# Optimization experiments

Hardware: AMD Instinct MI355X
Metric: run time of the kernel (lower is better)

The kernel has to match this reference:

```python
import jax, jax.numpy as jnp
import numpy as np

N_NODES = 100000
N_EDGES = 1600000
IN_F = 64
H1_F = 64
N_CLS = 16
NEG_SLOPE = 0.01  # F.leaky_relu default


def _sage_pool(x, src, dst, n_nodes, W_pool, b_pool, W_self, W_neigh, bias):
    """DGL SAGEConv with aggregator_type='pool'.
    msg = relu(x[src] @ W_pool + b_pool); pooled = max over in-edges per dst
    out = x @ W_self + pooled @ W_neigh + bias (empty segments pooled to 0)."""
    m = jax.nn.relu(x[src] @ W_pool + b_pool)                 # [E, d_in]
    pooled = jax.ops.segment_max(m, dst, num_segments=n_nodes)  # [N, d_in]
    deg = jax.ops.segment_sum(jnp.ones(dst.shape[0], x.dtype), dst,
                              num_segments=n_nodes)           # [N]
    pooled = jnp.where(deg[:, None] > 0, pooled, jnp.zeros((), x.dtype))
    return x @ W_self + pooled @ W_neigh + bias               # [N, d_out]


def setup_inputs() -> dict:
    key = jax.random.key(0)
    ks = jax.random.split(key, 12)
    sc_in = 1.0 / np.sqrt(IN_F)
    sc_h1 = 1.0 / np.sqrt(H1_F)
    inp = {
        "in_feat": jax.random.normal(ks[0], (N_NODES, IN_F), jnp.float32),
        "src": jax.random.randint(ks[1], (N_EDGES,), 0, N_NODES),
        "dst": jax.random.randint(ks[2], (N_EDGES,), 0, N_NODES),
        # layer 1 (in=64 -> out=64)
        "W_pool1": jax.random.normal(ks[3], (IN_F, IN_F), jnp.float32) * sc_in,
        "b_pool1": jnp.zeros((IN_F,), jnp.float32),
        "W_self1": jax.random.normal(ks[4], (IN_F, H1_F), jnp.float32) * sc_in,
        "W_neigh1": jax.random.normal(ks[5], (IN_F, H1_F), jnp.float32) * sc_in,
        "bias1": jnp.zeros((H1_F,), jnp.float32),
        # layer 2 (in=64 -> out=16)
        "W_pool2": jax.random.normal(ks[6], (H1_F, H1_F), jnp.float32) * sc_h1,
        "b_pool2": jnp.zeros((H1_F,), jnp.float32),
        "W_self2": jax.random.normal(ks[7], (H1_F, N_CLS), jnp.float32) * sc_h1,
        "W_neigh2": jax.random.normal(ks[8], (H1_F, N_CLS), jnp.float32) * sc_h1,
        "bias2": jnp.zeros((N_CLS,), jnp.float32),
    }
    return inp


def reference(in_feat, src, dst,
              W_pool1, b_pool1, W_self1, W_neigh1, bias1,
              W_pool2, b_pool2, W_self2, W_neigh2, bias2):
    n = in_feat.shape[0]
    h = _sage_pool(in_feat, src, dst, n, W_pool1, b_pool1, W_self1, W_neigh1, bias1)
    h = jnp.where(h >= 0, h, NEG_SLOPE * h)  # leaky_relu
    out = _sage_pool(h, src, dst, n, W_pool2, b_pool2, W_self2, W_neigh2, bias2)
    return out
```

## Files before the change

kernel.cpp:

```cpp
#include <hip/hip_runtime.h>
#include <cstddef>
#include <cstdint>

#define CAP 64
#define SCAP 40
#define CHUNK2 4096
#define PR 5632
#define HPR 2816

typedef _Float16 h2 __attribute__((ext_vector_type(2)));
typedef _Float16 f16x8 __attribute__((ext_vector_type(8)));
typedef float f32x4 __attribute__((ext_vector_type(4)));

static __device__ __forceinline__ h2 h2max(h2 a, h2 b) {
  return __builtin_elementwise_max(a, b);
}
static __device__ __forceinline__ h2 bch2(int u) { return __builtin_bit_cast(h2, u); }
static __device__ __forceinline__ int packrelu(float a, float b) {
  h2 t; t.x = (_Float16)fmaxf(a, 0.f); t.y = (_Float16)fmaxf(b, 0.f);
  return __builtin_bit_cast(int, t);
}
static __device__ __forceinline__ float fdot2f(h2 a, h2 b, float c) {
#if __has_builtin(__builtin_amdgcn_fdot2)
  return __builtin_amdgcn_fdot2(a, b, c, false);
#else
  return c + (float)a.x * (float)b.x + (float)a.y * (float)b.y;
#endif
}

static __device__ __forceinline__ void stageW64(h2* dstLds,
                                                const float* __restrict__ W,
                                                int tid) {
  #pragma unroll
  for (int it = 0; it < 2; it++) {
    int idx = it * 256 + tid;
    int kp = idx >> 4;
    int c4 = idx & 15;
    float4 a = ((const float4*)(W + (2 * kp) * 64))[c4];
    float4 b = ((const float4*)(W + (2 * kp + 1) * 64))[c4];
    h2 h0; h0.x = (_Float16)a.x; h0.y = (_Float16)b.x;
    h2 h1; h1.x = (_Float16)a.y; h1.y = (_Float16)b.y;
    h2 hv; hv.x = (_Float16)a.z; hv.y = (_Float16)b.z;
    h2 h3; h3.x = (_Float16)a.w; h3.y = (_Float16)b.w;
    int4 o = make_int4(__builtin_bit_cast(int, h0), __builtin_bit_cast(int, h1),
                       __builtin_bit_cast(int, hv), __builtin_bit_cast(int, h3));
    *(int4*)(dstLds + kp * 64 + c4 * 4) = o;
  }
}

static __device__ __forceinline__ f16x8 fragLd(const char* base, int row, int k0) {
  return *(const f16x8*)(base + ((row * 128 + k0 * 2) ^ ((row & 7) << 4)));
}
static __device__ __forceinline__ void stageWT(char* dstLds,
                                               const float* __restrict__ W,
                                               int tid) {
  #pragma unroll
  for (int it = 0; it < 4; it++) {
    int idx = it * 256 + tid;
    int k = idx >> 4;
    int c4 = idx & 15;
    float4 wv = ((const float4*)(W + k * 64))[c4];
    #pragma unroll
    for (int j = 0; j < 4; j++) {
      int col = c4 * 4 + j;
      float val = (j == 0) ? wv.x : (j == 1) ? wv.y : (j == 2) ? wv.z : wv.w;
      *(_Float16*)(dstLds + ((col * 128 + k * 2) ^ ((col & 7) << 4))) =
          (_Float16)val;
    }
  }
}

__global__ __launch_bounds__(256) void k_build(const int* __restrict__ src,
                                               const int* __restrict__ dst,
                                               unsigned int* __restrict__ pairs,
                                               int* __restrict__ cnt2,
                                               int E, int P, int NC,
                                               const float* __restrict__ X,
                                               const float* __restrict__ W,
                                               const float* __restrict__ bias,
                                               _Float16* __restrict__ Z, int n) {
  __shared__ __attribute__((aligned(16))) char smem[24576];
  int tid = threadIdx.x;
  if ((int)blockIdx.x < NC) {
    int* hcnt = (int*)smem;
    for (int p = tid; p < 512; p += 256) hcnt[p] = 0;
    __syncthreads();
    int chunk = blockIdx.x;
    int e0 = chunk * CHUNK2;
    unsigned int* pbase = pairs + (size_t)chunk * P * SCAP;
    #pragma unroll
    for (int k = 0; k < CHUNK2 / 256; k++) {
      int e = e0 + k * 256 + tid;
      if (e < E) {
        int d = dst[e], s = src[e];
        int p = d >> 8;
        int slot = atomicAdd(&hcnt[p], 1);
        if (slot < SCAP)
          pbase[p * SCAP + slot] = (unsigned)s | ((unsigned)(d & 255) << 17);
      }
    }
    __syncthreads();
    int* cbase = cnt2 + (size_t)chunk * P;
    for (int p = tid; p < P; p += 256) {
      int c = hcnt[p];
      cbase[p] = (c < SCAP) ? c : SCAP;
    }
    return;
  }
  h2* sW  = (h2*)smem;
  h2* sXT = (h2*)(smem + 8192);
  stageW64(sW, W, tid);
  int node0 = (blockIdx.x - NC) * 128;
  #pragma unroll
  for (int it = 0; it < 8; it++) {
    int idx = it * 256 + tid;
    int row = idx & 127, c4 = idx >> 7;
    int node = node0 + row;
    float4 v = make_float4(0.f, 0.f, 0.f, 0.f);
    if (node < n) v = ((const float4*)(X + (size_t)node * 64))[c4];
    h2 a; a.x = (_Float16)v.x; a.y = (_Float16)v.y;
    h2 d; d.x = (_Float16)v.z; d.y = (_Float16)v.w;
    sXT[(2 * c4 + 0) * 128 + row] = a;
    sXT[(2 * c4 + 1) * 128 + row] = d;
  }
  __syncthreads();
  int lane = tid & 63;
  int cg = tid >> 6;
  float acc0[16], acc1[16];
  #pragma unroll
  for (int c4 = 0; c4 < 4; c4++) {
    float4 bv = ((const float4*)bias)[cg * 4 + c4];
    acc0[c4 * 4 + 0] = bv.x; acc0[c4 * 4 + 1] = bv.y;
    acc0[c4 * 4 + 2] = bv.z; acc0[c4 * 4 + 3] = bv.w;
    acc1[c4 * 4 + 0] = bv.x; acc1[c4 * 4 + 1] = bv.y;
    acc1[c4 * 4 + 2] = bv.z; acc1[c4 * 4 + 3] = bv.w;
  }
  #pragma unroll 8
  for (int kp = 0; kp < 32; kp++) {
    h2 x0 = sXT[kp * 128 + lane];
    h2 x1 = sXT[kp * 128 + lane + 64];
    const int4* wq = (const int4*)(sW + kp * 64 + cg * 16);
    #pragma unroll
    for (int q4 = 0; q4 < 4; q4++) {
      int4 wv = wq[q4];
      h2 w0 = bch2(wv.x), w1 = bch2(wv.y), w2 = bch2(wv.z), w3 = bch2(wv.w);
      acc0[q4 * 4 + 0] = fdot2f(x0, w0, acc0[q4 * 4 + 0]);
      acc0[q4 * 4 + 1] = fdot2f(x0, w1, acc0[q4 * 4 + 1]);
      acc0[q4 * 4 + 2] = fdot2f(x0, w2, acc0[q4 * 4 + 2]);
      acc0[q4 * 4 + 3] = fdot2f(x0, w3, acc0[q4 * 4 + 3]);
      acc1[q4 * 4 + 0] = fdot2f(x1, w0, acc1[q4 * 4 + 0]);
      acc1[q4 * 4 + 1] = fdot2f(x1, w1, acc1[q4 * 4 + 1]);
      acc1[q4 * 4 + 2] = fdot2f(x1, w2, acc1[q4 * 4 + 2]);
      acc1[q4 * 4 + 3] = fdot2f(x1, w3, acc1[q4 * 4 + 3]);
    }
  }
  int nodeA = node0 + lane;
  int nodeB = node0 + lane + 64;
  if (nodeA < n) {
    int4 o0, o1;
    o0.x = packrelu(acc0[0], acc0[1]);   o0.y = packrelu(acc0[2], acc0[3]);
    o0.z = packrelu(acc0[4], acc0[5]);   o0.w = packrelu(acc0[6], acc0[7]);
    o1.x = packrelu(acc0[8], acc0[9]);   o1.y = packrelu(acc0[10], acc0[11]);
    o1.z = packrelu(acc0[12], acc0[13]); o1.w = packrelu(acc0[14], acc0[15]);
    char* rp = (char*)Z + (size_t)nodeA * 128 + cg * 32;
    ((int4*)rp)[0] = o0; ((int4*)rp)[1] = o1;
  }
  if (nodeB < n) {
    int4 o0, o1;
    o0.x = packrelu(acc1[0], acc1[1]);   o0.y = packrelu(acc1[2], acc1[3]);
    o0.z = packrelu(acc1[4], acc1[5]);   o0.w = packrelu(acc1[6], acc1[7]);
    o1.x = packrelu(acc1[8], acc1[9]);   o1.y = packrelu(acc1[10], acc1[11]);
    o1.z = packrelu(acc1[12], acc1[13]); o1.w = packrelu(acc1[14], acc1[15]);
    char* rp = (char*)Z + (size_t)nodeB * 128 + cg * 32;
    ((int4*)rp)[0] = o0; ((int4*)rp)[1] = o1;
  }
}

__global__ __launch_bounds__(256) void k_fill3(const unsigned int* __restrict__ pairs,
                                               const int* __restrict__ cnt2,
                                               int* __restrict__ rowcnt,
                                               int* __restrict__ bucket,
                                               int n, int NC, int P) {
  __shared__ int sbucket[128 * CAP];
  __shared__ int scnt[128];
  __shared__ int soff[256];
  __shared__ int scnt2[512];
  int tid = threadIdx.x;
  int p = blockIdx.x >> 1;
  int half = blockIdx.x & 1;
  if (tid < 128) scnt[tid] = 0;
  for (int c = tid; c < NC; c += 256) scnt2[c] = cnt2[(size_t)c * P + p];
  __syncthreads();
  int total = NC * SCAP;
  for (int t = tid; t < total; t += 256) {
    int chunk = t / SCAP;
    int slot = t - chunk * SCAP;
    if (slot < scnt2[chunk]) {
      unsigned int u = pairs[(size_t)chunk * P * SCAP + p * SCAP + slot];
      int dlow = (int)(u >> 17);
      if ((dlow >> 7) == half) {
        int s = (int)(u & 0x1FFFFu);
        int li = dlow & 127;
        int sl = atomicAdd(&scnt[li], 1);
        if (sl < CAP)
          sbucket[li * CAP + sl] = s;
      }
    }
  }
  __syncthreads();
  int c = 0;
  if (tid < 128) {
    c = scnt[tid];
    if (c > CAP) c = CAP;
  }
  int ca = (c + 3) & ~3;
  soff[tid] = (tid < 128) ? ca : 0;
  __syncthreads();
  #pragma unroll
  for (int off = 1; off < 256; off <<= 1) {
    int t = (tid >= off) ? soff[tid - off] : 0;
    __syncthreads();
    soff[tid] += t;
    __syncthreads();
  }
  if (tid < 128) {
    int local = soff[tid] - ca;
    int node = (p << 8) + (half << 7) + tid;
    int gbase = p * PR + half * HPR + local;
    if (node < n)
      rowcnt[node] = gbase | (c << 22);
    for (int j = 0; j < c; j += 4) {
      int4 v = *(const int4*)&sbucket[tid * CAP + j];
      *(int4*)&bucket[gbase + j] = v;
    }
  }
}

static __device__ __forceinline__ h2 gather_one(const char* zb,
                                                const int* __restrict__ bucket,
                                                int rc) {
  int c = rc >> 22;
  const int* bk = bucket + (rc & 0x3FFFFF);
  h2 acc = (h2)(_Float16)0;
  int j = 0;
  for (; j + 8 <= c; j += 8) {
    int4 a = *(const int4*)(bk + j);
    int4 d = *(const int4*)(bk + j + 4);
    int u0 = *(const int*)(zb + (size_t)a.x * 128);
    int u1 = *(const int*)(zb + (size_t)a.y * 128);
    int u2 = *(const int*)(zb + (size_t)a.z * 128);
    int u3 = *(const int*)(zb + (size_t)a.w * 128);
    int u4 = *(const int*)(zb + (size_t)d.x * 128);
    int u5 = *(const int*)(zb + (size_t)d.y * 128);
    int u6 = *(const int*)(zb + (size_t)d.z * 128);
    int u7 = *(const int*)(zb + (size_t)d.w * 128);
    h2 m0 = h2max(bch2(u0), bch2(u1));
    h2 m1 = h2max(bch2(u2), bch2(u3));
    h2 m2 = h2max(bch2(u4), bch2(u5));
    h2 m3 = h2max(bch2(u6), bch2(u7));
    acc = h2max(acc, h2max(h2max(m0, m1), h2max(m2, m3)));
  }
  if (j + 4 <= c) {
    int4 a = *(const int4*)(bk + j);
    int u0 = *(const int*)(zb + (size_t)a.x * 128);
    int u1 = *(const int*)(zb + (size_t)a.y * 128);
    int u2 = *(const int*)(zb + (size_t)a.z * 128);
    int u3 = *(const int*)(zb + (size_t)a.w * 128);
    acc = h2max(acc, h2max(h2max(bch2(u0), bch2(u1)), h2max(bch2(u2), bch2(u3))));
    j += 4;
  }
  if (j + 2 <= c) {
    int2 a = *(const int2*)(bk + j);
    int u0 = *(const int*)(zb + (size_t)a.x * 128);
    int u1 = *(const int*)(zb + (size_t)a.y * 128);
    acc = h2max(acc, h2max(bch2(u0), bch2(u1)));
    j += 2;
  }
  if (j < c) {
    int u0 = *(const int*)(zb + (size_t)bk[j] * 128);
    acc = h2max(acc, bch2(u0));
  }
  return acc;
}

__global__ __launch_bounds__(256) void k_gather2(const _Float16* __restrict__ Z,
                                                 const int* __restrict__ bucket,
                                                 const int* __restrict__ rowcnt,
                                                 _Float16* __restrict__ pooled, int n) {
  int t = blockIdx.x * 256 + threadIdx.x;
  int pairid = t >> 5;
  int sub = t & 31;
  int nA = pairid * 2;
  int nB = nA + 1;
  if (nA >= n) return;
  const char* zb = (const char*)Z + sub * 4;
  int rcA = rowcnt[nA];
  h2 accA, accB;
  if (nB < n) {
    int rcB = rowcnt[nB];
    accA = gather_one(zb, bucket, rcA);
    accB = gather_one(zb, bucket, rcB);
    *(int*)((char*)pooled + (size_t)nA * 128 + sub * 4) = __builtin_bit_cast(int, accA);
    *(int*)((char*)pooled + (size_t)nB * 128 + sub * 4) = __builtin_bit_cast(int, accB);
  } else {
    accA = gather_one(zb, bucket, rcA);
    *(int*)((char*)pooled + (size_t)nA * 128 + sub * 4) = __builtin_bit_cast(int, accA);
  }
}

__global__ __launch_bounds__(256) void k_hl(const float* __restrict__ X,
                                            const _Float16* __restrict__ P,
                                            const float* __restrict__ Ws,
                                            const float* __restrict__ Wn,
                                            const float* __restrict__ bias,
                                            const float* __restrict__ Wp2,
                                            const float* __restrict__ bp2,
                                            _Float16* __restrict__ H,
                                            _Float16* __restrict__ Z2, int n) {
  __shared__ __attribute__((aligned(16))) char sX[128 * 128];
  __shared__ __attribute__((aligned(16))) char sP[128 * 128];
  __shared__ __attribute__((aligned(16))) char sWsT[64 * 128];
  __shared__ __attribute__((aligned(16))) char sWnT[64 * 128];
  int tid = threadIdx.x;
  stageWT(sWsT, Ws, tid);
  stageWT(sWnT, Wn, tid);
  int node0 = blockIdx.x * 128;
  #pragma unroll
  for (int it = 0; it < 8; it++) {
    int idx = it * 256 + tid;
    int row = idx & 127, c4 = idx >> 7;
    int node = node0 + row;
    float4 v = make_float4(0.f, 0.f, 0.f, 0.f);
    if (node < n) v = ((const float4*)(X + (size_t)node * 64))[c4];
    h2 lo; lo.x = (_Float16)v.x; lo.y = (_Float16)v.y;
    h2 hi; hi.x = (_Float16)v.z; hi.y = (_Float16)v.w;
    int2 pk = make_int2(__builtin_bit_cast(int, lo), __builtin_bit_cast(int, hi));
    *(int2*)(sX + ((row * 128 + c4 * 8) ^ ((row & 7) << 4))) = pk;
  }
  #pragma unroll
  for (int it = 0; it < 4; it++) {
    int idx = it * 256 + tid;
    int row = idx & 127, q = idx >> 7;
    int node = node0 + row;
    int4 u = make_int4(0, 0, 0, 0);
    if (node < n) u = ((const int4*)((const char*)P + (size_t)node * 128))[q];
    *(int4*)(sP + ((row * 128 + q * 16) ^ ((row & 7) << 4))) = u;
  }
  __syncthreads();
  int l = tid & 63;
  int wv_ = tid >> 6;
  int wrow = wv_ * 32;
  int colq = l & 15;
  int kgrp = (l >> 4) * 8;
  f32x4 acc[2][4];
  #pragma unroll
  for (int m = 0; m < 2; m++)
    #pragma unroll
    for (int nt = 0; nt < 4; nt++) {
      float bv = bias[nt * 16 + colq];
      acc[m][nt] = (f32x4){bv, bv, bv, bv};
    }
  #pragma unroll
  for (int ks = 0; ks < 64; ks += 32) {
    f16x8 xa0 = fragLd(sX, wrow + colq, ks + kgrp);
    f16x8 xa1 = fragLd(sX, wrow + 16 + colq, ks + kgrp);
    f16x8 pa0 = fragLd(sP, wrow + colq, ks + kgrp);
    f16x8 pa1 = fragLd(sP, wrow + 16 + colq, ks + kgrp);
    #pragma unroll
    for (int nt = 0; nt < 4; nt++) {
      f16x8 bs = fragLd(sWsT, nt * 16 + colq, ks + kgrp);
      f16x8 bn = fragLd(sWnT, nt * 16 + colq, ks + kgrp);
      acc[0][nt] = __builtin_amdgcn_mfma_f32_16x16x32_f16(xa0, bs, acc[0][nt], 0, 0, 0);
      acc[1][nt] = __builtin_amdgcn_mfma_f32_16x16x32_f16(xa1, bs, acc[1][nt], 0, 0, 0);
      acc[0][nt] = __builtin_amdgcn_mfma_f32_16x16x32_f16(pa0, bn, acc[0][nt], 0, 0, 0);
      acc[1][nt] = __builtin_amdgcn_mfma_f32_16x16x32_f16(pa1, bn, acc[1][nt], 0, 0, 0);
    }
  }
  __syncthreads();
  int rbase = (l >> 4) * 4;
  #pragma unroll
  for (int m = 0; m < 2; m++)
    #pragma unroll
    for (int nt = 0; nt < 4; nt++)
      #pragma unroll
      for (int r = 0; r < 4; r++) {
        int nl = wrow + m * 16 + rbase + r;
        int col = nt * 16 + colq;
        float hv = acc[m][nt][r];
        hv = (hv >= 0.f) ? hv : 0.01f * hv;
        *(_Float16*)(sX + ((nl * 128 + col * 2) ^ ((nl & 7) << 4))) = (_Float16)hv;
      }
  stageWT(sWsT, Wp2, tid);
  __syncthreads();
  #pragma unroll
  for (int it = 0; it < 4; it++) {
    int idx = it * 256 + tid;
    int row = idx & 127, q = idx >> 7;
    int node = node0 + row;
    if (node < n) {
      int4 u = *(const int4*)(sX + ((row * 128 + q * 16) ^ ((row & 7) << 4)));
      ((int4*)((char*)H + (size_t)node * 128))[q] = u;
    }
  }
  f32x4 acc2[2][4];
  #pragma unroll
  for (int m = 0; m < 2; m++)
    #pragma unroll
    for (int nt = 0; nt < 4; nt++) {
      float bv = bp2[nt * 16 + colq];
      acc2[m][nt] = (f32x4){bv, bv, bv, bv};
    }
  #pragma unroll
  for (int ks = 0; ks < 64; ks += 32) {
    f16x8 ha0 = fragLd(sX, wrow + colq, ks + kgrp);
    f16x8 ha1 = fragLd(sX, wrow + 16 + colq, ks + kgrp);
    #pragma unroll
    for (int nt = 0; nt < 4; nt++) {
      f16x8 b = fragLd(sWsT, nt * 16 + colq, ks + kgrp);
      acc2[0][nt] = __builtin_amdgcn_mfma_f32_16x16x32_f16(ha0, b, acc2[0][nt], 0, 0, 0);
      acc2[1][nt] = __builtin_amdgcn_mfma_f32_16x16x32_f16(ha1, b, acc2[1][nt], 0, 0, 0);
    }
  }
  #pragma unroll
  for (int m = 0; m < 2; m++)
    #pragma unroll
    for (int nt = 0; nt < 4; nt++)
      #pragma unroll
      for (int r = 0; r < 4; r++) {
        int nl = wrow + m * 16 + rbase + r;
        int col = nt * 16 + colq;
        float zv = fmaxf(acc2[m][nt][r], 0.f);
        *(_Float16*)(sP + ((nl * 128 + col * 2) ^ ((nl & 7) << 4))) = (_Float16)zv;
      }
  __syncthreads();
  #pragma unroll
  for (int it = 0; it < 4; it++) {
    int idx = it * 256 + tid;
    int row = idx & 127, q = idx >> 7;
    int node = node0 + row;
    if (node < n) {
      int4 u = *(const int4*)(sP + ((row * 128 + q * 16) ^ ((row & 7) << 4)));
      ((int4*)((char*)Z2 + (size_t)node * 128))[q] = u;
    }
  }
}

__global__ __launch_bounds__(256) void k_gather_out(const _Float16* __restrict__ Z,
                                                    const int* __restrict__ bucket,
                                                    const int* __restrict__ rowcnt,
                                                    const _Float16* __restrict__ Hrow,
                                                    const float* __restrict__ Ws,
                                                    const float* __restrict__ Wn,
                                                    const float* __restrict__ bias,
                                                    float* __restrict__ OUT, int n) {
  __shared__ __attribute__((aligned(16))) h2 sWs[32 * 16];
  __shared__ __attribute__((aligned(16))) h2 sWn[32 * 16];
  __shared__ __attribute__((aligned(16))) h2 sH[8][32];
  __shared__ __attribute__((aligned(16))) h2 sP[8][32];
  __shared__ float sB[16];
  int tid = threadIdx.x;
  #pragma unroll
  for (int it = 0; it < 2; it++) {
    int idx = it * 256 + tid;
    int kp = idx >> 4, c = idx & 15;
    h2 t1, t2;
    t1.x = (_Float16)Ws[(2 * kp) * 16 + c];
    t1.y = (_Float16)Ws[(2 * kp + 1) * 16 + c];
    t2.x = (_Float16)Wn[(2 * kp) * 16 + c];
    t2.y = (_Float16)Wn[(2 * kp + 1) * 16 + c];
    sWs[kp * 16 + c] = t1;
    sWn[kp * 16 + c] = t2;
  }
  if (tid < 16) sB[tid] = bias[tid];
  int nodeBase = blockIdx.x * 8;
  if (tid < 64) {
    int nd = nodeBase + (tid >> 3);
    int q = tid & 7;
    int4 u = make_int4(0, 0, 0, 0);
    if (nd < n) u = ((const int4*)((const char*)Hrow + (size_t)nd * 128))[q];
    ((int4*)&sH[tid >> 3][0])[q] = u;
  }
  int en = tid >> 5;
  int node = nodeBase + en;
  int sub = tid & 31;
  h2 acc = (h2)(_Float16)0;
  if (node < n)
    acc = gather_one((const char*)Z + sub * 4, bucket, rowcnt[node]);
  sP[en][sub] = acc;
  __syncthreads();
  int col = tid & 15;
  int kh = (tid >> 4) & 1;
  float v = 0.f;
  #pragma unroll
  for (int j = 0; j < 16; j++) {
    int kp = kh * 16 + j;
    v = fdot2f(sH[en][kp], sWs[kp * 16 + col], v);
    v = fdot2f(sP[en][kp], sWn[kp * 16 + col], v);
  }
  v += __shfl_xor(v, 16);
  if (kh == 0 && node < n)
    OUT[(size_t)node * 16 + col] = v + sB[col];
}

extern "C" void kernel_launch(void* const* d_in, const int* in_sizes, int n_in,
                              void* d_out, int out_size, void* d_ws, size_t ws_size,
                              hipStream_t stream) {
  const float* X   = (const float*)d_in[0];
  const int*   src = (const int*)d_in[1];
  const int*   dst = (const int*)d_in[2];
  const float* Wp1 = (const float*)d_in[3];
  const float* bp1 = (const float*)d_in[4];
  const float* Ws1 = (const float*)d_in[5];
  const float* Wn1 = (const float*)d_in[6];
  const float* b1  = (const float*)d_in[7];
  const float* Wp2 = (const float*)d_in[8];
  const float* bp2 = (const float*)d_in[9];
  const float* Ws2 = (const float*)d_in[10];
  const float* Wn2 = (const float*)d_in[11];
  const float* b2  = (const float*)d_in[12];
  float* OUT = (float*)d_out;

  const int n = in_sizes[0] / 64;
  const int E = in_sizes[1];
  const int P = (n + 255) >> 8;
  const int NC = (E + CHUNK2 - 1) / CHUNK2;

  char* w = (char*)d_ws;
  auto alloc = [&](size_t bytes) -> char* {
    char* p = w;
    w += (bytes + 255) & ~(size_t)255;
    return p;
  };
  int*  rowcnt = (int*)alloc((size_t)n * 4);
  int*  bucket = (int*)alloc((size_t)P * PR * 4);
  int*  cnt2   = (int*)alloc((size_t)NC * P * 4);
  size_t pairs_b = (size_t)NC * P * SCAP * 4;
  size_t h_b     = (size_t)n * 64 * 2;
  char* ali = alloc(pairs_b > h_b ? pairs_b : h_b);
  unsigned int* pairs = (unsigned int*)ali;
  _Float16*     h16   = (_Float16*)ali;
  _Float16* zh     = (_Float16*)alloc((size_t)n * 64 * 2);
  _Float16* pooled = (_Float16*)alloc((size_t)n * 64 * 2);
  (void)ws_size; (void)n_in; (void)out_size;

  const int nbT  = (n + 127) / 128;
  const int nbG2 = (n * 16 + 255) / 256;
  const int nbG8 = (n + 7) / 8;

  k_build<<<NC + nbT, 256, 0, stream>>>(src, dst, pairs, cnt2, E, P, NC,
                                        X, Wp1, bp1, zh, n);
  k_fill3<<<2 * P, 256, 0, stream>>>(pairs, cnt2, rowcnt, bucket, n, NC, P);
  k_gather2<<<nbG2, 256, 0, stream>>>(zh, bucket, rowcnt, pooled, n);
  k_hl<<<nbT, 256, 0, stream>>>(X, pooled, Ws1, Wn1, b1, Wp2, bp2, h16, zh, n);
  k_gather_out<<<nbG8, 256, 0, stream>>>(zh, bucket, rowcnt, h16,
                                         Ws2, Wn2, b2, OUT, n);
}
```

Before: 166.2 us.

## Move layer-1 pool GEMM into fill kernel and compute it with MFMA

The X@W_pool1 projection moves out of the binning kernel and is co-scheduled with the bucket-fill kernel as extra blocks. It is also rewritten from packed fdot2 accumulation to MFMA 16x16x32 f16 using swizzled LDS tiles, with the result staged through LDS for coalesced stores. The aim is to shorten the edge-binning kernel, fill the fill kernel's grid with independent work, and cut ALU cost of the GEMM. Shared memory per block grows to 36KB, which may reduce occupancy for the fill blocks.

```diff
diff --git a/kernel.cpp b/kernel.cpp
--- a/kernel.cpp
+++ b/kernel.cpp
@@ -16,10 +16,6 @@
   return __builtin_elementwise_max(a, b);
 }
 static __device__ __forceinline__ h2 bch2(int u) { return __builtin_bit_cast(h2, u); }
-static __device__ __forceinline__ int packrelu(float a, float b) {
-  h2 t; t.x = (_Float16)fmaxf(a, 0.f); t.y = (_Float16)fmaxf(b, 0.f);
-  return __builtin_bit_cast(int, t);
-}
 static __device__ __forceinline__ float fdot2f(h2 a, h2 b, float c) {
 #if __has_builtin(__builtin_amdgcn_fdot2)
   return __builtin_amdgcn_fdot2(a, b, c, false);
@@ -28,26 +24,6 @@
 #endif
 }
 
-static __device__ __forceinline__ void stageW64(h2* dstLds,
-                                                const float* __restrict__ W,
-                                                int tid) {
-  #pragma unroll
-  for (int it = 0; it < 2; it++) {
-    int idx = it * 256 + tid;
-    int kp = idx >> 4;
-    int c4 = idx & 15;
-    float4 a = ((const float4*)(W + (2 * kp) * 64))[c4];
-    float4 b = ((const float4*)(W + (2 * kp + 1) * 64))[c4];
-    h2 h0; h0.x = (_Float16)a.x; h0.y = (_Float16)b.x;
-    h2 h1; h1.x = (_Float16)a.y; h1.y = (_Float16)b.y;
-    h2 hv; hv.x = (_Float16)a.z; hv.y = (_Float16)b.z;
-    h2 h3; h3.x = (_Float16)a.w; h3.y = (_Float16)b.w;
-    int4 o = make_int4(__builtin_bit_cast(int, h0), __builtin_bit_cast(int, h1),
-                       __builtin_bit_cast(int, hv), __builtin_bit_cast(int, h3));
-    *(int4*)(dstLds + kp * 64 + c4 * 4) = o;
-  }
-}
-
 static __device__ __forceinline__ f16x8 fragLd(const char* base, int row, int k0) {
   return *(const f16x8*)(base + ((row * 128 + k0 * 2) ^ ((row & 7) << 4)));
 }
@@ -70,47 +46,107 @@
   }
 }
 
-__global__ __launch_bounds__(256) void k_build(const int* __restrict__ src,
-                                               const int* __restrict__ dst,
-                                               unsigned int* __restrict__ pairs,
-                                               int* __restrict__ cnt2,
-                                               int E, int P, int NC,
-                                               const float* __restrict__ X,
-                                               const float* __restrict__ W,
-                                               const float* __restrict__ bias,
-                                               _Float16* __restrict__ Z, int n) {
-  __shared__ __attribute__((aligned(16))) char smem[24576];
+__global__ __launch_bounds__(256) void k_binscatter(const int* __restrict__ src,
+                                                    const int* __restrict__ dst,
+                                                    unsigned int* __restrict__ pairs,
+                                                    int* __restrict__ cnt2,
+                                                    int E, int P) {
+  __shared__ int hcnt[512];
   int tid = threadIdx.x;
-  if ((int)blockIdx.x < NC) {
-    int* hcnt = (int*)smem;
-    for (int p = tid; p < 512; p += 256) hcnt[p] = 0;
+  for (int p = tid; p < 512; p += 256) hcnt[p] = 0;
+  __syncthreads();
+  int chunk = blockIdx.x;
+  int e0 = chunk * CHUNK2;
+  unsigned int* pbase = pairs + (size_t)chunk * P * SCAP;
+  #pragma unroll
+  for (int k = 0; k < CHUNK2 / 256; k++) {
+    int e = e0 + k * 256 + tid;
+    if (e < E) {
+      int d = dst[e], s = src[e];
+      int p = d >> 8;
+      int slot = atomicAdd(&hcnt[p], 1);
+      if (slot < SCAP)
+        pbase[p * SCAP + slot] = (unsigned)s | ((unsigned)(d & 255) << 17);
+    }
+  }
+  __syncthreads();
+  int* cbase = cnt2 + (size_t)chunk * P;
+  for (int p = tid; p < P; p += 256) {
+    int c = hcnt[p];
+    cbase[p] = (c < SCAP) ? c : SCAP;
+  }
+}
+
+__global__ __launch_bounds__(256) void k_fill3z(const unsigned int* __restrict__ pairs,
+                                                const int* __restrict__ cnt2,
+                                                int* __restrict__ rowcnt,
+                                                int* __restrict__ bucket,
+                                                int n, int NC, int P,
+                                                const float* __restrict__ X,
+                                                const float* __restrict__ W,
+                                                const float* __restrict__ bias,
+                                                _Float16* __restrict__ Z) {
+  __shared__ __attribute__((aligned(16))) char smem[36864];
+  int tid = threadIdx.x;
+  if ((int)blockIdx.x < 2 * P) {
+    int* sbucket = (int*)smem;
+    int* scnt    = (int*)(smem + 32768);
+    int* soff    = (int*)(smem + 33280);
+    int* scnt2   = (int*)(smem + 34304);
+    int p = blockIdx.x >> 1;
+    int half = blockIdx.x & 1;
+    if (tid < 128) scnt[tid] = 0;
+    for (int c = tid; c < NC; c += 256) scnt2[c] = cnt2[(size_t)c * P + p];
     __syncthreads();
-    int chunk = blockIdx.x;
-    int e0 = chunk * CHUNK2;
-    unsigned int* pbase = pairs + (size_t)chunk * P * SCAP;
-    #pragma unroll
-    for (int k = 0; k < CHUNK2 / 256; k++) {
-      int e = e0 + k * 256 + tid;
-      if (e < E) {
-        int d = dst[e], s = src[e];
-        int p = d >> 8;
-        int slot = atomicAdd(&hcnt[p], 1);
-        if (slot < SCAP)
-          pbase[p * SCAP + slot] = (unsigned)s | ((unsigned)(d & 255) << 17);
+    int total = NC * SCAP;
+    for (int t = tid; t < total; t += 256) {
+      int chunk = t / SCAP;
+      int slot = t - chunk * SCAP;
+      if (slot < scnt2[chunk]) {
+        unsigned int u = pairs[(size_t)chunk * P * SCAP + p * SCAP + slot];
+        int dlow = (int)(u >> 17);
+        if ((dlow >> 7) == half) {
+          int s = (int)(u & 0x1FFFFu);
+          int li = dlow & 127;
+          int sl = atomicAdd(&scnt[li], 1);
+          if (sl < CAP)
+            sbucket[li * CAP + sl] = s;
+        }
       }
     }
     __syncthreads();
-    int* cbase = cnt2 + (size_t)chunk * P;
-    for (int p = tid; p < P; p += 256) {
-      int c = hcnt[p];
-      cbase[p] = (c < SCAP) ? c : SCAP;
+    int c = 0;
+    if (tid < 128) {
+      c = scnt[tid];
+      if (c > CAP) c = CAP;
+    }
+    int ca = (c + 3) & ~3;
+    soff[tid] = (tid < 128) ? ca : 0;
+    __syncthreads();
+    #pragma unroll
+    for (int off = 1; off < 256; off <<= 1) {
+      int t = (tid >= off) ? soff[tid - off] : 0;
+      __syncthreads();
+      soff[tid] += t;
+      __syncthreads();
+    }
+    if (tid < 128) {
+      int local = soff[tid] - ca;
+      int node = (p << 8) + (half << 7) + tid;
+      int gbase = p * PR + half * HPR + local;
+      if (node < n)
+        rowcnt[node] = gbase | (c << 22);
+      for (int j = 0; j < c; j += 4) {
+        int4 v = *(const int4*)&sbucket[tid * CAP + j];
+        *(int4*)&bucket[gbase + j] = v;
+      }
     }
     return;
   }
-  h2* sW  = (h2*)smem;
-  h2* sXT = (h2*)(smem + 8192);
-  stageW64(sW, W, tid);
-  int node0 = (blockIdx.x - NC) * 128;
+  char* sX  = smem;
+  char* sWT = smem + 16384;
+  stageWT(sWT, W, tid);
+  int node0 = ((int)blockIdx.x - 2 * P) * 128;
   #pragma unroll
   for (int it = 0; it < 8; it++) {
     int idx = it * 256 + tid;
@@ -118,120 +154,58 @@
     int node = node0 + row;
     float4 v = make_float4(0.f, 0.f, 0.f, 0.f);
     if (node < n) v = ((const float4*)(X + (size_t)node * 64))[c4];
-    h2 a; a.x = (_Float16)v.x; a.y = (_Float16)v.y;
-    h2 d; d.x = (_Float16)v.z; d.y = (_Float16)v.w;
-    sXT[(2 * c4 + 0) * 128 + row] = a;
-    sXT[(2 * c4 + 1) * 128 + row] = d;
-  }
-  __syncthreads();
-  int lane = tid & 63;
-  int cg = tid >> 6;
-  float acc0[16], acc1[16];
-  #pragma unroll
-  for (int c4 = 0; c4 < 4; c4++) {
-    float4 bv = ((const float4*)bias)[cg * 4 + c4];
-    acc0[c4 * 4 + 0] = bv.x; acc0[c4 * 4 + 1] = bv.y;
-    acc0[c4 * 4 + 2] = bv.z; acc0[c4 * 4 + 3] = bv.w;
-    acc1[c4 * 4 + 0] = bv.x; acc1[c4 * 4 + 1] = bv.y;
-    acc1[c4 * 4 + 2] = bv.z; acc1[c4 * 4 + 3] = bv.w;
-  }
-  #pragma unroll 8
-  for (int kp = 0; kp < 32; kp++) {
-    h2 x0 = sXT[kp * 128 + lane];
-    h2 x1 = sXT[kp * 128 + lane + 64];
-    const int4* wq = (const int4*)(sW + kp * 64 + cg * 16);
-    #pragma unroll
-    for (int q4 = 0; q4 < 4; q4++) {
-      int4 wv = wq[q4];
-      h2 w0 = bch2(wv.x), w1 = bch2(wv.y), w2 = bch2(wv.z), w3 = bch2(wv.w);
-      acc0[q4 * 4 + 0] = fdot2f(x0, w0, acc0[q4 * 4 + 0]);
-      acc0[q4 * 4 + 1] = fdot2f(x0, w1, acc0[q4 * 4 + 1]);
-      acc0[q4 * 4 + 2] = fdot2f(x0, w2, acc0[q4 * 4 + 2]);
-      acc0[q4 * 4 + 3] = fdot2f(x0, w3, acc0[q4 * 4 + 3]);
-      acc1[q4 * 4 + 0] = fdot2f(x1, w0, acc1[q4 * 4 + 0]);
-      acc1[q4 * 4 + 1] = fdot2f(x1, w1, acc1[q4 * 4 + 1]);
-      acc1[q4 * 4 + 2] = fdot2f(x1, w2, acc1[q4 * 4 + 2]);
-      acc1[q4 * 4 + 3] = fdot2f(x1, w3, acc1[q4 * 4 + 3]);
-    }
-  }
-  int nodeA = node0 + lane;
-  int nodeB = node0 + lane + 64;
-  if (nodeA < n) {
-    int4 o0, o1;
-    o0.x = packrelu(acc0[0], acc0[1]);   o0.y = packrelu(acc0[2], acc0[3]);
-    o0.z = packrelu(acc0[4], acc0[5]);   o0.w = packrelu(acc0[6], acc0[7]);
-    o1.x = packrelu(acc0[8], acc0[9]);   o1.y = packrelu(acc0[10], acc0[11]);
-    o1.z = packrelu(acc0[12], acc0[13]); o1.w = packrelu(acc0[14], acc0[15]);
-    char* rp = (char*)Z + (size_t)nodeA * 128 + cg * 32;
-    ((int4*)rp)[0] = o0; ((int4*)rp)[1] = o1;
-  }
-  if (nodeB < n) {
-    int4 o0, o1;
-    o0.x = packrelu(acc1[0], acc1[1]);   o0.y = packrelu(acc1[2], acc1[3]);
-    o0.z = packrelu(acc1[4], acc1[5]);   o0.w = packrelu(acc1[6], acc1[7]);
-    o1.x = packrelu(acc1[8], acc1[9]);   o1.y = packrelu(acc1[10], acc1[11]);
-    o1.z = packrelu(acc1[12], acc1[13]); o1.w = packrelu(acc1[14], acc1[15]);
-    char* rp = (char*)Z + (size_t)nodeB * 128 + cg * 32;
-    ((int4*)rp)[0] = o0; ((int4*)rp)[1] = o1;
-  }
-}
-
-__global__ __launch_bounds__(256) void k_fill3(const unsigned int* __restrict__ pairs,
-                                               const int* __restrict__ cnt2,
-                                               int* __restrict__ rowcnt,
-                                               int* __restrict__ bucket,
-                                               int n, int NC, int P) {
-  __shared__ int sbucket[128 * CAP];
-  __shared__ int scnt[128];
-  __shared__ int soff[256];
-  __shared__ int scnt2[512];
-  int tid = threadIdx.x;
-  int p = blockIdx.x >> 1;
-  int half = blockIdx.x & 1;
-  if (tid < 128) scnt[tid] = 0;
-  for (int c = tid; c < NC; c += 256) scnt2[c] = cnt2[(size_t)c * P + p];
-  __syncthreads();
-  int total = NC * SCAP;
-  for (int t = tid; t < total; t += 256) {
-    int chunk = t / SCAP;
-    int slot = t - chunk * SCAP;
-    if (slot < scnt2[chunk]) {
-      unsigned int u = pairs[(size_t)chunk * P * SCAP + p * SCAP + slot];
-      int dlow = (int)(u >> 17);
-      if ((dlow >> 7) == half) {
-        int s = (int)(u & 0x1FFFFu);
-        int li = dlow & 127;
-        int sl = atomicAdd(&scnt[li], 1);
-        if (sl < CAP)
-          sbucket[li * CAP + sl] = s;
+    h2 lo; lo.x = (_Float16)v.x; lo.y = (_Float16)v.y;
+    h2 hi; hi.x = (_Float16)v.z; hi.y = (_Float16)v.w;
+    int2 pk = make_int2(__builtin_bit_cast(int, lo), __builtin_bit_cast(int, hi));
+    *(int2*)(sX + ((row * 128 + c4 * 8) ^ ((row & 7) << 4))) = pk;
+  }
+  __syncthreads();
+  int l = tid & 63;
+  int wv_ = tid >> 6;
+  int wrow = wv_ * 32;
+  int colq = l & 15;
+  int kgrp = (l >> 4) * 8;
+  f32x4 acc[2][4];
+  #pragma unroll
+  for (int m = 0; m < 2; m++)
+    #pragma unroll
+    for (int nt = 0; nt < 4; nt++) {
+      float bv = bias[nt * 16 + colq];
+      acc[m][nt] = (f32x4){bv, bv, bv, bv};
+    }
+  #pragma unroll
+  for (int ks = 0; ks < 64; ks += 32) {
+    f16x8 xa0 = fragLd(sX, wrow + colq, ks + kgrp);
+    f16x8 xa1 = fragLd(sX, wrow + 16 + colq, ks + kgrp);
+    #pragma unroll
+    for (int nt = 0; nt < 4; nt++) {
+      f16x8 b = fragLd(sWT, nt * 16 + colq, ks + kgrp);
+      acc[0][nt] = __builtin_amdgcn_mfma_f32_16x16x32_f16(xa0, b, acc[0][nt], 0, 0, 0);
+      acc[1][nt] = __builtin_amdgcn_mfma_f32_16x16x32_f16(xa1, b, acc[1][nt], 0, 0, 0);
+    }
+  }
+  __syncthreads();
+  int rbase = (l >> 4) * 4;
+  #pragma unroll
+  for (int m = 0; m < 2; m++)
+    #pragma unroll
+    for (int nt = 0; nt < 4; nt++)
+      #pragma unroll
+      for (int r = 0; r < 4; r++) {
+        int nl = wrow + m * 16 + rbase + r;
+        int col = nt * 16 + colq;
+        float zv = fmaxf(acc[m][nt][r], 0.f);
+        *(_Float16*)(sX + ((nl * 128 + col * 2) ^ ((nl & 7) << 4))) = (_Float16)zv;
       }
-    }
-  }
-  __syncthreads();
-  int c = 0;
-  if (tid < 128) {
-    c = scnt[tid];
-    if (c > CAP) c = CAP;
-  }
-  int ca = (c + 3) & ~3;
-  soff[tid] = (tid < 128) ? ca : 0;
-  __syncthreads();
-  #pragma unroll
-  for (int off = 1; off < 256; off <<= 1) {
-    int t = (tid >= off) ? soff[tid - off] : 0;
-    __syncthreads();
-    soff[tid] += t;
-    __syncthreads();
-  }
-  if (tid < 128) {
-    int local = soff[tid] - ca;
-    int node = (p << 8) + (half << 7) + tid;
-    int gbase = p * PR + half * HPR + local;
-    if (node < n)
-      rowcnt[node] = gbase | (c << 22);
-    for (int j = 0; j < c; j += 4) {
-      int4 v = *(const int4*)&sbucket[tid * CAP + j];
-      *(int4*)&bucket[gbase + j] = v;
+  __syncthreads();
+  #pragma unroll
+  for (int it = 0; it < 4; it++) {
+    int idx = it * 256 + tid;
+    int row = idx & 127, q = idx >> 7;
+    int node = node0 + row;
+    if (node < n) {
+      int4 u = *(const int4*)(sX + ((row * 128 + q * 16) ^ ((row & 7) << 4)));
+      ((int4*)((char*)Z + (size_t)node * 128))[q] = u;
     }
   }
 }
@@ -547,9 +521,9 @@
   const int nbG2 = (n * 16 + 255) / 256;
   const int nbG8 = (n + 7) / 8;
 
-  k_build<<<NC + nbT, 256, 0, stream>>>(src, dst, pairs, cnt2, E, P, NC,
-                                        X, Wp1, bp1, zh, n);
-  k_fill3<<<2 * P, 256, 0, stream>>>(pairs, cnt2, rowcnt, bucket, n, NC, P);
+  k_binscatter<<<NC, 256, 0, stream>>>(src, dst, pairs, cnt2, E, P);
+  k_fill3z<<<2 * P + nbT, 256, 0, stream>>>(pairs, cnt2, rowcnt, bucket,
+                                            n, NC, P, X, Wp1, bp1, zh);
   k_gather2<<<nbG2, 256, 0, stream>>>(zh, bucket, rowcnt, pooled, n);
   k_hl<<<nbT, 256, 0, stream>>>(X, pooled, Ws1, Wn1, b1, Wp2, bp2, h16, zh, n);
   k_gather_out<<<nbG8, 256, 0, stream>>>(zh, bucket, rowcnt, h16,
```

Measured after the change: 160.0 us. -3.7%, faster.
